# Performance work log

Hardware: AMD Instinct MI355X
Metric: run time of the kernel (lower is better)

The kernel has to match this reference:

```python
import jax, jax.numpy as jnp
import numpy as np

HEADS = 4
DIM_HEAD = 32
SCALE = DIM_HEAD ** -0.5


def setup_inputs() -> dict:
    key = jax.random.key(0)
    k1, k2, k3 = jax.random.split(key, 3)
    B, C, H, W = 4, 128, 64, 64
    inner = HEADS * DIM_HEAD  # 128
    x = jax.random.normal(k1, (B, C, H, W), dtype=jnp.float32)
    # 1x1 conv weights == channel-mixing matrices [out_ch, in_ch]
    w_qkv = jax.random.normal(k2, (inner * 3, C), dtype=jnp.float32) * (C ** -0.5)
    w_proj = jax.random.normal(k3, (C, inner), dtype=jnp.float32) * (inner ** -0.5)
    b_proj = jnp.zeros((C,), dtype=jnp.float32)
    return {"x": x, "w_qkv": w_qkv, "w_proj": w_proj, "b_proj": b_proj}


def reference(x, w_qkv, w_proj, b_proj):
    b, c, h, w = x.shape
    n = h * w
    # 1x1 conv = per-pixel matmul over channels
    qkv = jnp.einsum('bchw,oc->bohw', x, w_qkv)  # [B, 3*inner, H, W]
    q, k, v = jnp.split(qkv, 3, axis=1)

    def to_heads(t):
        # [B, inner, H, W] -> [B, heads, HW, dim_head]
        return t.reshape(b, HEADS, DIM_HEAD, n).transpose(0, 1, 3, 2)

    q = to_heads(q) * SCALE
    k = to_heads(k)
    v = to_heads(v)
    # scores [B, heads, HW, HW]; softmax is max-stabilized (matches torch amax-subtract)
    scores = jnp.einsum('bhnd,bhmd->bhnm', q, k)
    attn = jax.nn.softmax(scores, axis=-1)
    out = jnp.einsum('bhnm,bhmd->bhnd', attn, v)  # [B, heads, HW, dim_head]
    out = out.transpose(0, 1, 3, 2).reshape(b, HEADS * DIM_HEAD, h, w)
    return jnp.einsum('bchw,oc->bohw', out, w_proj) + b_proj[None, :, None, None]
```

## Files before the change

### kernel.cpp

```cpp
#include <hip/hip_runtime.h>

typedef _Float16 f16;
typedef unsigned short u16;
typedef __attribute__((ext_vector_type(8))) f16 f16x8;
typedef __attribute__((ext_vector_type(4))) f16 f16x4;
typedef __attribute__((ext_vector_type(4))) float floatx4;
typedef __attribute__((ext_vector_type(2))) __fp16 h2;

union pk4 { h2 h[2]; f16x4 v; };

#define NPIX 4096
#define KT   128
#define NT   (NPIX / KT)
#define VROW 136

__global__ __launch_bounds__(256) void qkv_mfma(
    const float* __restrict__ x, const float* __restrict__ w,
    f16* __restrict__ qh, f16* __restrict__ kh, f16* __restrict__ vth)
{
    __shared__ f16 wlds[64 * 136];
    const int tid  = threadIdx.x;
    const int wave = tid >> 6;
    const int lane = tid & 63;
    const int quad = lane >> 4;
    const int l16  = lane & 15;
    const int pbase = blockIdx.x * 64;
    const int y     = blockIdx.y;
    const int b     = blockIdx.z;

#pragma unroll
    for (int i = 0; i < 8; ++i) {
        int idx = i * 256 + tid;
        int o = idx >> 5, ch = idx & 31;
        float4 wv = *(const float4*)(w + (size_t)(y * 64 + o) * 128 + ch * 4);
        f16x4 h; h[0] = (f16)wv.x; h[1] = (f16)wv.y; h[2] = (f16)wv.z; h[3] = (f16)wv.w;
        *(f16x4*)&wlds[o * 136 + ch * 4] = h;
    }
    __syncthreads();

    const float* xb = x + (size_t)b * 128 * NPIX;
    const int type = y >> 1;

    if (type < 2) {
        const int p_row = pbase + wave * 16 + l16;
        f16x8 af[4];
#pragma unroll
        for (int kc = 0; kc < 4; ++kc) {
            const int c0 = kc * 32 + quad * 8;
#pragma unroll
            for (int j = 0; j < 8; ++j)
                af[kc][j] = (f16)xb[(size_t)(c0 + j) * NPIX + p_row];
        }
        floatx4 acc[4];
#pragma unroll
        for (int n = 0; n < 4; ++n) acc[n] = floatx4{0.f, 0.f, 0.f, 0.f};
#pragma unroll
        for (int n = 0; n < 4; ++n)
#pragma unroll
            for (int kc = 0; kc < 4; ++kc) {
                f16x8 bf = *(const f16x8*)&wlds[(n * 16 + l16) * 136 + kc * 32 + quad * 8];
                acc[n] = __builtin_amdgcn_mfma_f32_16x16x32_f16(af[kc], bf, acc[n], 0, 0, 0);
            }
        const float qs = (type == 0) ? 0.17677669529663687f * 1.4426950408889634f : 1.0f;
        f16* dst = (type == 0) ? qh : kh;
#pragma unroll
        for (int n = 0; n < 4; ++n) {
            const int og   = y * 64 + n * 16 + l16;
            const int head = (og >> 5) & 3;
            const int d    = og & 31;
            f16* base = dst + (size_t)(b * 4 + head) * NPIX * 32;
#pragma unroll
            for (int r = 0; r < 4; ++r) {
                const int p = pbase + wave * 16 + quad * 4 + r;
                base[(size_t)p * 32 + d] = (f16)(acc[n][r] * qs);
            }
        }
    } else {
        const int p_col = pbase + wave * 16 + l16;
        f16x8 bf[4];
#pragma unroll
        for (int kc = 0; kc < 4; ++kc) {
            const int c0 = kc * 32 + quad * 8;
#pragma unroll
            for (int j = 0; j < 8; ++j)
                bf[kc][j] = (f16)xb[(size_t)(c0 + j) * NPIX + p_col];
        }
        floatx4 acc[4];
#pragma unroll
        for (int m = 0; m < 4; ++m) acc[m] = floatx4{0.f, 0.f, 0.f, 0.f};
#pragma unroll
        for (int m = 0; m < 4; ++m)
#pragma unroll
            for (int kc = 0; kc < 4; ++kc) {
                f16x8 af = *(const f16x8*)&wlds[(m * 16 + l16) * 136 + kc * 32 + quad * 8];
                acc[m] = __builtin_amdgcn_mfma_f32_16x16x32_f16(af, bf[kc], acc[m], 0, 0, 0);
            }
#pragma unroll
        for (int m = 0; m < 4; ++m)
#pragma unroll
            for (int r = 0; r < 4; ++r) {
                const int og   = y * 64 + m * 16 + quad * 4 + r;
                const int head = (og >> 5) & 3;
                const int d    = og & 31;
                vth[((size_t)(b * 4 + head) * 32 + d) * NPIX + p_col] = (f16)acc[m][r];
            }
    }
}

#define ATTN_STEP(BUF, KF, KFN, TNXT)                                          \
{                                                                              \
                    \
    if ((TNXT) < NT) {                                                         \
        _Pragma("unroll")                                                      \
        for (int t = 0; t < 8; ++t)                                            \
            KFN[t] = *(const f16x8*)(kp + (size_t)((TNXT) * KT + t * 16) * 32);\
    }                                                                          \
         \
    int4 nv0, nv1;                                                             \
    if ((TNXT) < NT) {                                                         \
        const int4* vs = (const int4*)(vrow + (TNXT) * KT);                    \
        nv0 = vs[vcc]; nv1 = vs[vcc + 1];                                      \
    }                                                                          \
                                        \
    f16x4 vf[8][2];                                                            \
    _Pragma("unroll")                                                          \
    for (int c = 0; c < 8; ++c) {                                              \
        _Pragma("unroll")                                                      \
        for (int dh = 0; dh < 2; ++dh)                                         \
            vf[c][dh] = *(const f16x4*)&vlds[BUF][(dh * 16 + l16) * VROW + c * 16 + quad * 4]; \
    }                                                                          \
                     \
    floatx4 st0[8], st1[8];                                                    \
    _Pragma("unroll")                                                          \
    for (int t = 0; t < 8; ++t) {                                              \
        floatx4 z = {0.f, 0.f, 0.f, 0.f};                                      \
        st0[t] = __builtin_amdgcn_mfma_f32_16x16x32_f16(KF[t], qB[0], z, 0, 0, 0); \
    }                                                                          \
    _Pragma("unroll")                                                          \
    for (int t = 0; t < 8; ++t) {                                              \
        floatx4 z = {0.f, 0.f, 0.f, 0.f};                                      \
        st1[t] = __builtin_amdgcn_mfma_f32_16x16x32_f16(KF[t], qB[1], z, 0, 0, 0); \
    }                                                                          \
           \
    f16x4 pf0[8], pf1[8];                                                      \
    float ls0 = 0.f, ls1 = 0.f;                                                \
    _Pragma("unroll")                                                          \
    for (int c = 0; c < 8; ++c) {                                              \
        float e0 = __builtin_amdgcn_exp2f(st0[c][0]);                          \
        float e1 = __builtin_amdgcn_exp2f(st0[c][1]);                          \
        float e2 = __builtin_amdgcn_exp2f(st0[c][2]);                          \
        float e3 = __builtin_amdgcn_exp2f(st0[c][3]);                          \
        pk4 u;                                                                 \
        u.h[0] = __builtin_amdgcn_cvt_pkrtz(e0, e1);                           \
        u.h[1] = __builtin_amdgcn_cvt_pkrtz(e2, e3);                           \
        pf0[c] = u.v;                                                          \
        ls0 = __builtin_amdgcn_fdot2(u.h[0], one2, ls0, false);                \
        ls0 = __builtin_amdgcn_fdot2(u.h[1], one2, ls0, false);                \
    }                                                                          \
              \
    _Pragma("unroll")                                                          \
    for (int c = 0; c < 8; ++c) {                                              \
        oacc[0][0] = __builtin_amdgcn_mfma_f32_16x16x16f16(pf0[c], vf[c][0], oacc[0][0], 0, 0, 0); \
        oacc[0][1] = __builtin_amdgcn_mfma_f32_16x16x16f16(pf0[c], vf[c][1], oacc[0][1], 0, 0, 0); \
        float e0 = __builtin_amdgcn_exp2f(st1[c][0]);                          \
        float e1 = __builtin_amdgcn_exp2f(st1[c][1]);                          \
        float e2 = __builtin_amdgcn_exp2f(st1[c][2]);                          \
        float e3 = __builtin_amdgcn_exp2f(st1[c][3]);                          \
        pk4 u;                                                                 \
        u.h[0] = __builtin_amdgcn_cvt_pkrtz(e0, e1);                           \
        u.h[1] = __builtin_amdgcn_cvt_pkrtz(e2, e3);                           \
        pf1[c] = u.v;                                                          \
        ls1 = __builtin_amdgcn_fdot2(u.h[0], one2, ls1, false);                \
        ls1 = __builtin_amdgcn_fdot2(u.h[1], one2, ls1, false);                \
    }                                                                          \
    lsum[0] += ls0; lsum[1] += ls1;                                            \
    _Pragma("unroll")                                                          \
    for (int c = 0; c < 8; ++c) {                                              \
        oacc[1][0] = __builtin_amdgcn_mfma_f32_16x16x16f16(pf1[c], vf[c][0], oacc[1][0], 0, 0, 0); \
        oacc[1][1] = __builtin_amdgcn_mfma_f32_16x16x16f16(pf1[c], vf[c][1], oacc[1][1], 0, 0, 0); \
    }                                                                          \
           \
    if ((TNXT) < NT) {                                                         \
        *(int4*)&vlds[(BUF) ^ 1][voff]     = nv0;                              \
        *(int4*)&vlds[(BUF) ^ 1][voff + 8] = nv1;                              \
    }                                                                          \
    __syncthreads();                                                           \
}

__global__ __launch_bounds__(256, 2) void attn_kernel(
    const f16* __restrict__ qh, const f16* __restrict__ kh,
    const f16* __restrict__ vth, f16* __restrict__ att)
{
    __shared__ f16 vlds[2][32 * VROW];

    const int tid  = threadIdx.x;
    const int wave = tid >> 6;
    const int lane = tid & 63;
    const int quad = lane >> 4;
    const int l16  = lane & 15;
    const int bh   = blockIdx.y;
    const int qbase = blockIdx.x * 128 + wave * 32;

    const f16* kb = kh + (size_t)bh * NPIX * 32;
    const f16* vb = vth + (size_t)bh * 32 * NPIX;
    const f16* kp = kb + (size_t)l16 * 32 + quad * 8;

    const int vr = tid >> 3, vcc = (tid & 7) * 2;
    const int voff = vr * VROW + vcc * 8;
    const f16* vrow = vb + (size_t)vr * NPIX;

    const h2 one2 = {(__fp16)1.0f, (__fp16)1.0f};

    f16x8 qB[2];
#pragma unroll
    for (int h = 0; h < 2; ++h)
        qB[h] = *(const f16x8*)(qh + ((size_t)bh * NPIX + qbase + h * 16 + l16) * 32 + quad * 8);

    floatx4 oacc[2][2];
#pragma unroll
    for (int h = 0; h < 2; ++h)
#pragma unroll
        for (int dh = 0; dh < 2; ++dh) oacc[h][dh] = floatx4{0.f, 0.f, 0.f, 0.f};
    float lsum[2] = {0.f, 0.f};

    f16x8 kfA[8], kfB[8];
    {
        const int4* vs = (const int4*)vrow;
        int4 a = vs[vcc], b2 = vs[vcc + 1];
        *(int4*)&vlds[0][voff]     = a;
        *(int4*)&vlds[0][voff + 8] = b2;
    }
#pragma unroll
    for (int t = 0; t < 8; ++t)
        kfA[t] = *(const f16x8*)(kp + (size_t)(t * 16) * 32);
    __syncthreads();

    for (int it = 0; it < NT / 2; ++it) {
        const int t0 = it * 2;
        ATTN_STEP(0, kfA, kfB, t0 + 1);
        ATTN_STEP(1, kfB, kfA, t0 + 2);
    }

#pragma unroll
    for (int h = 0; h < 2; ++h) {
        float l = lsum[h];
        l += __shfl_xor(l, 16);
        l += __shfl_xor(l, 32);
        const float inv = 1.0f / l;
#pragma unroll
        for (int r = 0; r < 4; ++r) {
            const float invr = __shfl(inv, quad * 4 + r);
            const int q = qbase + h * 16 + quad * 4 + r;
            f16* ob = att + ((size_t)bh * NPIX + q) * 32;
            ob[l16]      = (f16)(oacc[h][0][r] * invr);
            ob[16 + l16] = (f16)(oacc[h][1][r] * invr);
        }
    }
}

__global__ __launch_bounds__(256) void proj_mfma(
    const f16* __restrict__ att, const float* __restrict__ wp,
    const float* __restrict__ bp, float* __restrict__ out)
{
    __shared__ f16 wplds[128 * 136];
    __shared__ float bplds[128];
    const int tid  = threadIdx.x;
    const int wave = tid >> 6;
    const int lane = tid & 63;
    const int quad = lane >> 4;
    const int l16  = lane & 15;
    const int pbase = blockIdx.x * 64;
    const int b     = blockIdx.y;

    if (tid < 128) bplds[tid] = bp[tid];
#pragma unroll
    for (int i = 0; i < 16; ++i) {
        int idx = i * 256 + tid;
        int o = idx >> 5, ch = idx & 31;
        float4 wv = *(const float4*)(wp + (size_t)o * 128 + ch * 4);
        f16x4 h; h[0] = (f16)wv.x; h[1] = (f16)wv.y; h[2] = (f16)wv.z; h[3] = (f16)wv.w;
        *(f16x4*)&wplds[o * 136 + ch * 4] = h;
    }
    __syncthreads();

    const f16* ab = att + (size_t)b * 4 * NPIX * 32;
    const int p_col = pbase + wave * 16 + l16;
    f16x8 bf[4];
#pragma unroll
    for (int kc = 0; kc < 4; ++kc)
        bf[kc] = *(const f16x8*)(ab + ((size_t)kc * NPIX + p_col) * 32 + quad * 8);

    floatx4 acc[8];
#pragma unroll
    for (int m = 0; m < 8; ++m) acc[m] = floatx4{0.f, 0.f, 0.f, 0.f};
#pragma unroll
    for (int m = 0; m < 8; ++m)
#pragma unroll
        for (int kc = 0; kc < 4; ++kc) {
            f16x8 af = *(const f16x8*)&wplds[(m * 16 + l16) * 136 + kc * 32 + quad * 8];
            acc[m] = __builtin_amdgcn_mfma_f32_16x16x32_f16(af, bf[kc], acc[m], 0, 0, 0);
        }

#pragma unroll
    for (int m = 0; m < 8; ++m)
#pragma unroll
        for (int r = 0; r < 4; ++r) {
            const int o = m * 16 + quad * 4 + r;
            out[((size_t)b * 128 + o) * NPIX + p_col] = acc[m][r] + bplds[o];
        }
}

extern "C" void kernel_launch(void* const* d_in, const int* in_sizes, int n_in,
                              void* d_out, int out_size, void* d_ws, size_t ws_size,
                              hipStream_t stream)
{
    const float* x      = (const float*)d_in[0];
    const float* w_qkv  = (const float*)d_in[1];
    const float* w_proj = (const float*)d_in[2];
    const float* b_proj = (const float*)d_in[3];
    float* out = (float*)d_out;

    char* ws = (char*)d_ws;
    f16* qh  = (f16*)(ws);
    f16* kh  = (f16*)(ws + (4u << 20));
    f16* vth = (f16*)(ws + (8u << 20));
    f16* att = (f16*)(ws + (12u << 20));

    qkv_mfma<<<dim3(64, 6, 4), 256, 0, stream>>>(x, w_qkv, qh, kh, vth);
    attn_kernel<<<dim3(32, 16, 1), 256, 0, stream>>>(qh, kh, vth, att);
    proj_mfma<<<dim3(64, 4, 1), 256, 0, stream>>>(att, w_proj, b_proj, out);
}
```

Before: 125.5 us.

## Pre-transpose input to pixel-major fp16 and split projection work across more blocks

Adds a transpose kernel that turns x into a pixel-major fp16 buffer, so the QKV kernel loads 16-byte vectors instead of doing strided scalar fp32 gathers, and the input is converted once rather than six times. The transposed buffer reuses the attention-output workspace region, which is safe because it is consumed before attention writes there. The projection kernel now gives each block 32 pixels and each wave half of the output channels, doubling the grid to raise occupancy. The cost is an extra launch plus an extra read and write of the fp16 input.

```diff
diff --git a/kernel.cpp b/kernel.cpp
--- a/kernel.cpp
+++ b/kernel.cpp
@@ -14,8 +14,36 @@
 #define NT   (NPIX / KT)
 #define VROW 136
 
+__global__ __launch_bounds__(256) void xpose(
+    const float* __restrict__ x, f16* __restrict__ xt)
+{
+    __shared__ f16 t[16 * 136];
+    const int tid = threadIdx.x;
+    const int pbase = blockIdx.x * 16;
+    const int b = blockIdx.y;
+    const float* xb = x + (size_t)b * 128 * NPIX;
+
+#pragma unroll
+    for (int i = 0; i < 2; ++i) {
+        int idx = i * 256 + tid;
+        int c = idx >> 2, p4 = (idx & 3) * 4;
+        float4 v = *(const float4*)(xb + (size_t)c * NPIX + pbase + p4);
+        t[(p4 + 0) * 136 + c] = (f16)v.x;
+        t[(p4 + 1) * 136 + c] = (f16)v.y;
+        t[(p4 + 2) * 136 + c] = (f16)v.z;
+        t[(p4 + 3) * 136 + c] = (f16)v.w;
+    }
+    __syncthreads();
+
+    f16* ob = xt + ((size_t)b * NPIX + pbase) * 128;
+    {
+        int p = tid >> 4, c8 = (tid & 15) * 8;
+        *(f16x8*)(ob + (size_t)p * 128 + c8) = *(const f16x8*)&t[p * 136 + c8];
+    }
+}
+
 __global__ __launch_bounds__(256) void qkv_mfma(
-    const float* __restrict__ x, const float* __restrict__ w,
+    const f16* __restrict__ xt, const float* __restrict__ w,
     f16* __restrict__ qh, f16* __restrict__ kh, f16* __restrict__ vth)
 {
     __shared__ f16 wlds[64 * 136];
@@ -38,28 +66,25 @@
     }
     __syncthreads();
 
-    const float* xb = x + (size_t)b * 128 * NPIX;
     const int type = y >> 1;
+    const int p_row = pbase + wave * 16 + l16;
+
+    f16x8 xf[4];
+#pragma unroll
+    for (int kc = 0; kc < 4; ++kc)
+        xf[kc] = *(const f16x8*)(xt + ((size_t)b * NPIX + p_row) * 128 + kc * 32 + quad * 8);
+
+    floatx4 acc[4];
+#pragma unroll
+    for (int n = 0; n < 4; ++n) acc[n] = floatx4{0.f, 0.f, 0.f, 0.f};
 
     if (type < 2) {
-        const int p_row = pbase + wave * 16 + l16;
-        f16x8 af[4];
-#pragma unroll
-        for (int kc = 0; kc < 4; ++kc) {
-            const int c0 = kc * 32 + quad * 8;
-#pragma unroll
-            for (int j = 0; j < 8; ++j)
-                af[kc][j] = (f16)xb[(size_t)(c0 + j) * NPIX + p_row];
-        }
-        floatx4 acc[4];
-#pragma unroll
-        for (int n = 0; n < 4; ++n) acc[n] = floatx4{0.f, 0.f, 0.f, 0.f};
 #pragma unroll
         for (int n = 0; n < 4; ++n)
 #pragma unroll
             for (int kc = 0; kc < 4; ++kc) {
                 f16x8 bf = *(const f16x8*)&wlds[(n * 16 + l16) * 136 + kc * 32 + quad * 8];
-                acc[n] = __builtin_amdgcn_mfma_f32_16x16x32_f16(af[kc], bf, acc[n], 0, 0, 0);
+                acc[n] = __builtin_amdgcn_mfma_f32_16x16x32_f16(xf[kc], bf, acc[n], 0, 0, 0);
             }
         const float qs = (type == 0) ? 0.17677669529663687f * 1.4426950408889634f : 1.0f;
         f16* dst = (type == 0) ? qh : kh;
@@ -76,24 +101,12 @@
             }
         }
     } else {
-        const int p_col = pbase + wave * 16 + l16;
-        f16x8 bf[4];
-#pragma unroll
-        for (int kc = 0; kc < 4; ++kc) {
-            const int c0 = kc * 32 + quad * 8;
-#pragma unroll
-            for (int j = 0; j < 8; ++j)
-                bf[kc][j] = (f16)xb[(size_t)(c0 + j) * NPIX + p_col];
-        }
-        floatx4 acc[4];
-#pragma unroll
-        for (int m = 0; m < 4; ++m) acc[m] = floatx4{0.f, 0.f, 0.f, 0.f};
 #pragma unroll
         for (int m = 0; m < 4; ++m)
 #pragma unroll
             for (int kc = 0; kc < 4; ++kc) {
                 f16x8 af = *(const f16x8*)&wlds[(m * 16 + l16) * 136 + kc * 32 + quad * 8];
-                acc[m] = __builtin_amdgcn_mfma_f32_16x16x32_f16(af, bf[kc], acc[m], 0, 0, 0);
+                acc[m] = __builtin_amdgcn_mfma_f32_16x16x32_f16(af, xf[kc], acc[m], 0, 0, 0);
             }
 #pragma unroll
         for (int m = 0; m < 4; ++m)
@@ -102,7 +115,7 @@
                 const int og   = y * 64 + m * 16 + quad * 4 + r;
                 const int head = (og >> 5) & 3;
                 const int d    = og & 31;
-                vth[((size_t)(b * 4 + head) * 32 + d) * NPIX + p_col] = (f16)acc[m][r];
+                vth[((size_t)(b * 4 + head) * 32 + d) * NPIX + p_row] = (f16)acc[m][r];
             }
     }
 }
@@ -269,7 +282,7 @@
     const int lane = tid & 63;
     const int quad = lane >> 4;
     const int l16  = lane & 15;
-    const int pbase = blockIdx.x * 64;
+    const int pbase = blockIdx.x * 32;
     const int b     = blockIdx.y;
 
     if (tid < 128) bplds[tid] = bp[tid];
@@ -284,29 +297,30 @@
     __syncthreads();
 
     const f16* ab = att + (size_t)b * 4 * NPIX * 32;
-    const int p_col = pbase + wave * 16 + l16;
+    const int p_col = pbase + (wave & 1) * 16 + l16;
+    const int mbase = (wave >> 1) * 4;
     f16x8 bf[4];
 #pragma unroll
     for (int kc = 0; kc < 4; ++kc)
         bf[kc] = *(const f16x8*)(ab + ((size_t)kc * NPIX + p_col) * 32 + quad * 8);
 
-    floatx4 acc[8];
-#pragma unroll
-    for (int m = 0; m < 8; ++m) acc[m] = floatx4{0.f, 0.f, 0.f, 0.f};
-#pragma unroll
-    for (int m = 0; m < 8; ++m)
+    floatx4 acc[4];
+#pragma unroll
+    for (int mi = 0; mi < 4; ++mi) acc[mi] = floatx4{0.f, 0.f, 0.f, 0.f};
+#pragma unroll
+    for (int mi = 0; mi < 4; ++mi)
 #pragma unroll
         for (int kc = 0; kc < 4; ++kc) {
-            f16x8 af = *(const f16x8*)&wplds[(m * 16 + l16) * 136 + kc * 32 + quad * 8];
-            acc[m] = __builtin_amdgcn_mfma_f32_16x16x32_f16(af, bf[kc], acc[m], 0, 0, 0);
+            f16x8 af = *(const f16x8*)&wplds[((mbase + mi) * 16 + l16) * 136 + kc * 32 + quad * 8];
+            acc[mi] = __builtin_amdgcn_mfma_f32_16x16x32_f16(af, bf[kc], acc[mi], 0, 0, 0);
         }
 
 #pragma unroll
-    for (int m = 0; m < 8; ++m)
+    for (int mi = 0; mi < 4; ++mi)
 #pragma unroll
         for (int r = 0; r < 4; ++r) {
-            const int o = m * 16 + quad * 4 + r;
-            out[((size_t)b * 128 + o) * NPIX + p_col] = acc[m][r] + bplds[o];
+            const int o = (mbase + mi) * 16 + quad * 4 + r;
+            out[((size_t)b * 128 + o) * NPIX + p_col] = acc[mi][r] + bplds[o];
         }
 }
 
@@ -325,8 +339,10 @@
     f16* kh  = (f16*)(ws + (4u << 20));
     f16* vth = (f16*)(ws + (8u << 20));
     f16* att = (f16*)(ws + (12u << 20));
-
-    qkv_mfma<<<dim3(64, 6, 4), 256, 0, stream>>>(x, w_qkv, qh, kh, vth);
+    f16* xt  = (f16*)(ws + (12u << 20));
+
+    xpose<<<dim3(256, 4, 1), 256, 0, stream>>>(x, xt);
+    qkv_mfma<<<dim3(64, 6, 4), 256, 0, stream>>>(xt, w_qkv, qh, kh, vth);
     attn_kernel<<<dim3(32, 16, 1), 256, 0, stream>>>(qh, kh, vth, att);
-    proj_mfma<<<dim3(64, 4, 1), 256, 0, stream>>>(att, w_proj, b_proj, out);
-}
+    proj_mfma<<<dim3(128, 4, 1), 256, 0, stream>>>(att, w_proj, b_proj, out);
+}
```

New measurement: 130.4 us. 3.8% more time.
